# Kernel tuning notes

Measured on AMD Instinct MI355X. Metric: run time of the kernel, lower is better.

## Reference

```python
import jax, jax.numpy as jnp
import numpy as np

B, S, D, H = 4, 2048, 512, 4
HD = D // H
EPS = 1e-5


def layer_norm(x, gamma, beta):
    mu = jnp.mean(x, axis=-1, keepdims=True)
    var = jnp.mean(jnp.square(x - mu), axis=-1, keepdims=True)
    return (x - mu) * jax.lax.rsqrt(var + EPS) * gamma + beta


def setup_inputs() -> dict:
    key = jax.random.key(0)
    ks = jax.random.split(key, 16)
    s_in = 1.0 / np.sqrt(D)
    s_ex = 1.0 / np.sqrt(2 * D)
    return {
        "input_states": jax.random.normal(ks[0], (B, S, D), jnp.float32),
        "positions": jax.random.normal(ks[1], (B, S, 3), jnp.float32),
        "W_expand": jax.random.uniform(ks[2], (D, 2 * D), jnp.float32, -s_in, s_in),
        "b_expand": jax.random.uniform(ks[3], (2 * D,), jnp.float32, -s_in, s_in),
        "W_squeeze": jax.random.uniform(ks[4], (2 * D, D), jnp.float32, -s_ex, s_ex),
        "b_squeeze": jax.random.uniform(ks[5], (D,), jnp.float32, -s_ex, s_ex),
        "gamma": jnp.ones((D,), jnp.float32),
        "beta": jnp.zeros((D,), jnp.float32),
        "Wq": jax.random.uniform(ks[6], (D, D), jnp.float32, -s_in, s_in),
        "bq": jax.random.uniform(ks[7], (D,), jnp.float32, -s_in, s_in),
        "Wk": jax.random.uniform(ks[8], (D, D), jnp.float32, -s_in, s_in),
        "bk": jax.random.uniform(ks[9], (D,), jnp.float32, -s_in, s_in),
        "Wv": jax.random.uniform(ks[10], (D, D), jnp.float32, -s_in, s_in),
        "bv": jax.random.uniform(ks[11], (D,), jnp.float32, -s_in, s_in),
        "alpha": jnp.float32(0.1),
    }


def reference(input_states, positions, W_expand, b_expand, W_squeeze, b_squeeze,
              gamma, beta, Wq, bq, Wk, bk, Wv, bv, alpha):
    # FFN (expand -> relu -> squeeze) + residual + LayerNorm
    h = jax.nn.relu(input_states @ W_expand + b_expand)
    squeezed = h @ W_squeeze + b_squeeze
    se = layer_norm(input_states + squeezed, gamma, beta)

    # q/k/v projections, split heads: [B,H,S,HD]
    q = (se @ Wq + bq).reshape(B, S, H, HD).transpose(0, 2, 1, 3)
    k = (se @ Wk + bk).reshape(B, S, H, HD).transpose(0, 2, 1, 3)
    v = (se @ Wv + bv).reshape(B, S, H, HD).transpose(0, 2, 1, 3)

    scores = jnp.einsum('bhid,bhjd->bhij', q, k) / np.sqrt(HD)

    # squared pairwise distance bias: ||pi||^2 + ||pj||^2 - 2 pi.pj, broadcast over heads
    sq = jnp.sum(positions * positions, axis=-1)  # [B,S]
    dist2 = sq[:, :, None] + sq[:, None, :] - 2.0 * jnp.einsum('bic,bjc->bij', positions, positions)
    dist2 = jnp.maximum(dist2, 0.0)
    scores = scores - alpha * dist2[:, None, :, :]

    w = jax.nn.softmax(scores, axis=-1)
    ctx = jnp.einsum('bhij,bhjd->bhid', w, v)
    ctx = ctx.transpose(0, 2, 1, 3).reshape(B, S, D)

    # same LayerNorm params reused (self.norm applied twice in original)
    return layer_norm(se + ctx, gamma, beta)
```

## Files before the change

kernel.cpp:

```cpp
#include <hip/hip_runtime.h>

typedef __bf16 bf16_t;
typedef __attribute__((ext_vector_type(8))) __bf16 bf16x8;
typedef __attribute__((ext_vector_type(4))) __bf16 bf16x4;
typedef __attribute__((ext_vector_type(4))) float f32x4;
typedef __attribute__((ext_vector_type(16))) float f32x16;

constexpr int Bc = 4, Sc = 2048, Dc = 512, Hc = 4, HDc = 128;
constexpr int Mrows = Bc * Sc;

__device__ inline void gl2lds(const void* g, void* l) {
  __builtin_amdgcn_global_load_lds(
      (__attribute__((address_space(1))) void*)g,
      (__attribute__((address_space(3))) void*)l, 16, 0, 0);
}

__global__ __launch_bounds__(256) void prep_k(
    const float* __restrict__ X, bf16_t* __restrict__ xb,
    const float* __restrict__ pos, const float* __restrict__ alphap,
    float* __restrict__ pos2,
    const float* __restrict__ We, bf16_t* __restrict__ wtE,
    const float* __restrict__ Ws, bf16_t* __restrict__ wtS,
    const float* __restrict__ Wq, const float* __restrict__ Wk,
    const float* __restrict__ Wv, bf16_t* __restrict__ wtQKV) {
  const int bid = blockIdx.x;
  if (bid < 2048) {
    const long i = ((long)bid * 256 + threadIdx.x) * 8;
    const float4 a = *(const float4*)(X + i);
    const float4 c = *(const float4*)(X + i + 4);
    bf16x8 o;
    o[0] = (bf16_t)a.x; o[1] = (bf16_t)a.y; o[2] = (bf16_t)a.z; o[3] = (bf16_t)a.w;
    o[4] = (bf16_t)c.x; o[5] = (bf16_t)c.y; o[6] = (bf16_t)c.z; o[7] = (bf16_t)c.w;
    *(bf16x8*)(xb + i) = o;
    return;
  }
  if (bid < 2080) {
    const float aL = alphap[0] * 1.4426950408889634f;
    const int i = (bid - 2048) * 256 + threadIdx.x;
    const float x = pos[(long)i * 3], y = pos[(long)i * 3 + 1], z = pos[(long)i * 3 + 2];
    float4 o; o.x = x; o.y = y; o.z = z; o.w = -aL * (x * x + y * y + z * z);
    *(float4*)(pos2 + (long)i * 4) = o;
    return;
  }
  __shared__ float tile[32][33];
  const float* src; bf16_t* dst; int K, N, local;
  if (bid < 2592)      { src = We; dst = wtE; K = 512;  N = 1024; local = bid - 2080; }
  else if (bid < 3104) { src = Ws; dst = wtS; K = 1024; N = 512;  local = bid - 2592; }
  else if (bid < 3360) { src = Wq; dst = wtQKV;          K = 512; N = 512; local = bid - 3104; }
  else if (bid < 3616) { src = Wk; dst = wtQKV + 262144; K = 512; N = 512; local = bid - 3360; }
  else                 { src = Wv; dst = wtQKV + 524288; K = 512; N = 512; local = bid - 3616; }
  const int nb = N / 32;
  const int n0 = (local % nb) * 32, k0 = (local / nb) * 32;
  const int tx = threadIdx.x & 31, ty = threadIdx.x >> 5;
#pragma unroll
  for (int i = 0; i < 4; i++)
    tile[ty + i * 8][tx] = src[(long)(k0 + ty + i * 8) * N + n0 + tx];
  __syncthreads();
#pragma unroll
  for (int i = 0; i < 4; i++)
    dst[(long)(n0 + ty + i * 8) * K + k0 + tx] = (bf16_t)tile[tx][ty + i * 8];
}

template <int OMODE, int TN, int NB>
__global__ __launch_bounds__(256, (TN == 128) ? 2 : 3) void gemm128_k(
    const bf16_t* __restrict__ A, const bf16_t* __restrict__ Bt,
    const float* __restrict__ bias0, const float* __restrict__ bias1,
    const float* __restrict__ bias2, void* __restrict__ out0,
    void* __restrict__ out1, void* __restrict__ out2, int N, int K) {
  __shared__ bf16_t As[2][128 * 64];
  __shared__ bf16_t Bs[2][TN * 64];
  constexpr int MT = (TN == 128) ? 4 : 2;
  constexpr int BI = (TN == 128) ? 4 : 2;
  constexpr int MW = (TN == 128) ? 64 : 32;
  const int t = threadIdx.x;
  const int p = blockIdx.x;
  const int slot = p >> 3;
  const int by = (p & 7) + 8 * (slot / NB);
  const int bx = slot % NB;
  const int n0 = bx * TN, m0 = by * 128;
  const int lane = t & 63, wave = t >> 6;
  const int quad = lane >> 4, ln = lane & 15;
  const int wm = (TN == 128) ? (wave >> 1) : wave;
  const int wn = (TN == 128) ? (wave & 1) : 0;
  const int l8 = lane >> 3, g = lane & 7;
  const bf16_t* aseg = A + (long)(m0 + wave * 32 + l8) * K + (g ^ l8) * 8;
  const bf16_t* bseg = Bt + (long)(n0 + wave * (BI * 8) + l8) * K + (g ^ l8) * 8;
  auto stage = [&](int buf, int k0) {
#pragma unroll
    for (int i = 0; i < 4; i++)
      gl2lds(aseg + (long)i * 8 * K + k0, &As[buf][(wave * 32 + i * 8) * 64]);
#pragma unroll
    for (int i = 0; i < BI; i++)
      gl2lds(bseg + (long)i * 8 * K + k0, &Bs[buf][(wave * BI * 8 + i * 8) * 64]);
  };
  f32x4 acc[MT][4] = {};
  stage(0, 0);
  const int niter = K / 64;
  for (int it = 0; it < niter; it++) {
    const int cur = it & 1;
    __syncthreads();
    if (it + 1 < niter) stage(1 - cur, (it + 1) * 64);
#pragma unroll
    for (int kc = 0; kc < 2; kc++) {
      bf16x8 af[MT], bfr[4];
#pragma unroll
      for (int mt = 0; mt < MT; mt++)
        af[mt] = *(const bf16x8*)&As[cur][(wm * MW + mt * 16 + ln) * 64 +
                                          (((kc * 4 + quad) ^ (ln & 7)) * 8)];
#pragma unroll
      for (int nt = 0; nt < 4; nt++)
        bfr[nt] = *(const bf16x8*)&Bs[cur][(wn * 64 + nt * 16 + ln) * 64 +
                                           (((kc * 4 + quad) ^ (ln & 7)) * 8)];
#pragma unroll
      for (int mt = 0; mt < MT; mt++)
#pragma unroll
        for (int nt = 0; nt < 4; nt++)
          acc[mt][nt] = __builtin_amdgcn_mfma_f32_16x16x32_bf16(af[mt], bfr[nt],
                                                                acc[mt][nt], 0, 0, 0);
    }
  }
#pragma unroll
  for (int nt = 0; nt < 4; nt++) {
    const int gcol = n0 + wn * 64 + nt * 16 + ln;
    if constexpr (OMODE == 0 || OMODE == 1) {
      const float bv = bias0[gcol];
      bf16_t* o = (bf16_t*)out0;
#pragma unroll
      for (int mt = 0; mt < MT; mt++)
#pragma unroll
        for (int r = 0; r < 4; r++) {
          const int grow = m0 + wm * MW + mt * 16 + quad * 4 + r;
          float vv = acc[mt][nt][r] + bv;
          if constexpr (OMODE == 0) vv = vv > 0.f ? vv : 0.f;
          o[(long)grow * N + gcol] = (bf16_t)vv;
        }
    } else {
      const int which = gcol >> 9, n = gcol & 511;
      const int hh = n >> 7, hd = n & 127;
      const float bv = (which == 0 ? bias0 : which == 1 ? bias1 : bias2)[n];
      bf16_t* o = (bf16_t*)(which == 0 ? out0 : which == 1 ? out1 : out2);
#pragma unroll
      for (int mt = 0; mt < MT; mt++)
#pragma unroll
        for (int r = 0; r < 4; r++) {
          const int grow = m0 + wm * MW + mt * 16 + quad * 4 + r;
          const int b = grow >> 11, s = grow & 2047;
          const float vv = acc[mt][nt][r] + bv;
          long idx;
          if (which == 0) {
            idx = ((long)((b * Hc + hh) * Sc + s)) * HDc + hd;
          } else if (which == 1) {
            const int tt = s >> 6, kh = (s >> 5) & 1, key = s & 31;
            const int c = hd >> 4, lk = key + 32 * ((hd >> 3) & 1), j = hd & 7;
            idx = ((((long)((b * Hc + hh) * 32 + tt) * 2 + kh) * 8 + c) * 64 + lk) * 8 + j;
          } else {
            const int tt = s >> 6, ht2 = hd >> 5, kc = (s & 63) >> 4;
            const int lk = (hd & 31) + 32 * ((s >> 3) & 1), j = s & 7;
            idx = ((((long)((b * Hc + hh) * 32 + tt) * 4 + ht2) * 4 + kc) * 64 + lk) * 8 + j;
          }
          o[idx] = (bf16_t)vv;
        }
    }
  }
}

template <int AF32, int OF32>
__global__ __launch_bounds__(256) void ln_k(const void* __restrict__ xa,
                                            const bf16_t* __restrict__ xb,
                                            const float* __restrict__ gamma,
                                            const float* __restrict__ beta,
                                            void* __restrict__ out) {
  const int wave = threadIdx.x >> 6, lane = threadIdx.x & 63;
  const long row = (long)blockIdx.x * 4 + wave;
  const int col0 = lane * 8;
  float vv[8];
  float s = 0.f, s2 = 0.f;
  const bf16x8 vb = *(const bf16x8*)(xb + row * Dc + col0);
  if constexpr (AF32) {
    const float* a = (const float*)xa + row * Dc + col0;
    const float4 a0 = *(const float4*)a;
    const float4 a1 = *(const float4*)(a + 4);
    const float xs[8] = {a0.x, a0.y, a0.z, a0.w, a1.x, a1.y, a1.z, a1.w};
#pragma unroll
    for (int j = 0; j < 8; j++) vv[j] = xs[j] + (float)vb[j];
  } else {
    const bf16x8 va = *(const bf16x8*)((const bf16_t*)xa + row * Dc + col0);
#pragma unroll
    for (int j = 0; j < 8; j++) vv[j] = (float)va[j] + (float)vb[j];
  }
#pragma unroll
  for (int j = 0; j < 8; j++) { s += vv[j]; s2 += vv[j] * vv[j]; }
#pragma unroll
  for (int off = 1; off < 64; off <<= 1) {
    s += __shfl_xor(s, off, 64);
    s2 += __shfl_xor(s2, off, 64);
  }
  const float mu = s * (1.f / Dc);
  const float var = s2 * (1.f / Dc) - mu * mu;
  const float rstd = rsqrtf(var + 1e-5f);
  const float4 g0 = *(const float4*)(gamma + col0);
  const float4 g1 = *(const float4*)(gamma + col0 + 4);
  const float4 b0 = *(const float4*)(beta + col0);
  const float4 b1 = *(const float4*)(beta + col0 + 4);
  const float gs[8] = {g0.x, g0.y, g0.z, g0.w, g1.x, g1.y, g1.z, g1.w};
  const float bs[8] = {b0.x, b0.y, b0.z, b0.w, b1.x, b1.y, b1.z, b1.w};
  if constexpr (OF32) {
    float* o = (float*)out + row * Dc + col0;
    float4 o0, o1;
    o0.x = (vv[0] - mu) * rstd * gs[0] + bs[0];
    o0.y = (vv[1] - mu) * rstd * gs[1] + bs[1];
    o0.z = (vv[2] - mu) * rstd * gs[2] + bs[2];
    o0.w = (vv[3] - mu) * rstd * gs[3] + bs[3];
    o1.x = (vv[4] - mu) * rstd * gs[4] + bs[4];
    o1.y = (vv[5] - mu) * rstd * gs[5] + bs[5];
    o1.z = (vv[6] - mu) * rstd * gs[6] + bs[6];
    o1.w = (vv[7] - mu) * rstd * gs[7] + bs[7];
    *(float4*)o = o0; *(float4*)(o + 4) = o1;
  } else {
    bf16x8 ob;
#pragma unroll
    for (int j = 0; j < 8; j++) ob[j] = (bf16_t)((vv[j] - mu) * rstd * gs[j] + bs[j]);
    *(bf16x8*)((bf16_t*)out + row * Dc + col0) = ob;
  }
}

__global__ __launch_bounds__(256, 2) void attn_k(const bf16_t* __restrict__ q,
                                                 const bf16_t* __restrict__ Kg,
                                                 const bf16_t* __restrict__ Vg,
                                                 const float* __restrict__ pos2,
                                                 const float* __restrict__ alphap,
                                                 bf16_t* __restrict__ ctx) {
  __shared__ bf16_t Ks[2][8192];
  __shared__ bf16_t Vts[2][8192];
  __shared__ float pk4[2][64][4];
  __shared__ bf16_t Ps[4][1024];
  __shared__ float RsD[4][32];
  const int t = threadIdx.x;
  const int p = blockIdx.x;
  const int qt = (p >> 3) & 31;
  const int gg = (p & 7) + 8 * (p >> 8);
  const int h = gg & 3, b = gg >> 2;
  const int q0 = qt * 64;
  const int wave = t >> 6, lane = t & 63;
  const int l31 = lane & 31, hb = lane >> 5;
  const int rh = wave & 1, kh = wave >> 1;
  const float l2e = 1.4426950408889634f;
  const float scale_l2 = l2e * 0.08838834764831845f;
  const float aL = alphap[0] * l2e;

  bf16x8 qf[8];
  const long qrow = (long)((b * Hc + h) * Sc + q0 + rh * 32 + l31);
#pragma unroll
  for (int c = 0; c < 8; c++)
    qf[c] = *(const bf16x8*)(q + qrow * HDc + c * 16 + hb * 8);
  float pqx, pqy, pqz;
  {
    const float4 pv = *(const float4*)(pos2 + (long)(b * Sc + q0 + rh * 32 + l31) * 4);
    pqx = 2.f * aL * pv.x; pqy = 2.f * aL * pv.y; pqz = 2.f * aL * pv.z;
  }

  const bf16_t* ktile = Kg + (long)((b * Hc + h) * 32) * 8192 + lane * 8;
  const bf16_t* vtile = Vg + (long)((b * Hc + h) * 32) * 8192 + lane * 8;
  const float* pcur = pos2 + (long)b * Sc * 4 + lane * 4;
  auto stage = [&](int buf) {
#pragma unroll
    for (int i = 0; i < 4; i++)
      gl2lds(ktile + (wave * 4 + i) * 512, &Ks[buf][(wave * 4 + i) * 512]);
#pragma unroll
    for (int i = 0; i < 4; i++)
      gl2lds(vtile + (wave * 4 + i) * 512, &Vts[buf][(wave * 4 + i) * 512]);
    if (wave == 0) gl2lds(pcur, &pk4[buf][0][0]);
  };
  stage(0);
  ktile += 8192; vtile += 8192; pcur += 256;

  float rsl = 0.f;
  f32x16 accT[4] = {};
  bf16_t* pwbase = &Ps[wave][l31 * 8 + 4 * hb];

  for (int kt = 0; kt < Sc / 64; kt++) {
    const int cur = kt & 1;
    __syncthreads();
    if (kt < Sc / 64 - 1) {
      stage(1 - cur);
      ktile += 8192; vtile += 8192; pcur += 256;
    }
    f32x16 sacc = {};
#pragma unroll
    for (int c = 0; c < 8; c++) {
      const bf16x8 kf = *(const bf16x8*)&Ks[cur][(kh * 8 + c) * 512 + lane * 8];
      sacc = __builtin_amdgcn_mfma_f32_32x32x16_bf16(kf, qf[c], sacc, 0, 0, 0);
    }
#pragma unroll
    for (int g2 = 0; g2 < 4; g2++) {
      bf16x4 pq4;
#pragma unroll
      for (int r0 = 0; r0 < 4; r0++) {
        const int kp = r0 + 4 * hb + 8 * g2;
        const float4 pv = *(const float4*)&pk4[cur][kh * 32 + kp][0];
        const float bias = __builtin_fmaf(pqx, pv.x,
                           __builtin_fmaf(pqy, pv.y,
                           __builtin_fmaf(pqz, pv.z, pv.w)));
        const float pe = __builtin_amdgcn_exp2f(
            __builtin_fmaf(sacc[g2 * 4 + r0], scale_l2, bias));
        rsl += pe;
        pq4[r0] = (bf16_t)pe;
      }
      *(bf16x4*)(pwbase + (g2 >> 1) * 512 + (g2 & 1) * 256) = pq4;
    }
    const bf16x8 pf0 = *(const bf16x8*)&Ps[wave][lane * 8];
    const bf16x8 pf1 = *(const bf16x8*)&Ps[wave][512 + lane * 8];
#pragma unroll
    for (int ht = 0; ht < 4; ht++) {
      const bf16x8 v0 = *(const bf16x8*)&Vts[cur][(ht * 4 + kh * 2 + 0) * 512 + lane * 8];
      accT[ht] = __builtin_amdgcn_mfma_f32_32x32x16_bf16(v0, pf0, accT[ht], 0, 0, 0);
      const bf16x8 v1 = *(const bf16x8*)&Vts[cur][(ht * 4 + kh * 2 + 1) * 512 + lane * 8];
      accT[ht] = __builtin_amdgcn_mfma_f32_32x32x16_bf16(v1, pf1, accT[ht], 0, 0, 0);
    }
  }
  __syncthreads();

  rsl += __shfl_xor(rsl, 32, 64);
  if (hb == 0) RsD[wave][l31] = rsl;
  float* Oc = (float*)&Ks[0][0];
  if (kh == 1) {
#pragma unroll
    for (int ht = 0; ht < 4; ht++)
#pragma unroll
      for (int r = 0; r < 16; r++) {
        const int hdp = (r & 3) + 8 * (r >> 2) + 4 * hb;
        Oc[(ht * 32 + hdp) * 64 + rh * 32 + l31] = accT[ht][r];
      }
  }
  __syncthreads();
  if (kh == 0) {
    const float rinv = 1.f / (RsD[wave][l31] + RsD[wave + 2][l31]);
    const long orow = (long)(b * Sc + q0 + rh * 32 + l31);
#pragma unroll
    for (int ht = 0; ht < 4; ht++)
#pragma unroll
      for (int g2 = 0; g2 < 4; g2++) {
        bf16x4 ov;
#pragma unroll
        for (int r0 = 0; r0 < 4; r0++) {
          const int hdp = r0 + 8 * g2 + 4 * hb;
          ov[r0] = (bf16_t)((accT[ht][g2 * 4 + r0] +
                             Oc[(ht * 32 + hdp) * 64 + rh * 32 + l31]) * rinv);
        }
        *(bf16x4*)(ctx + orow * Dc + h * HDc + ht * 32 + 8 * g2 + 4 * hb) = ov;
      }
  }
}

constexpr size_t SQB_OFF = 0;
constexpr size_t SEB_OFF = 8388608;
constexpr size_t Q_OFF = 16777216;
constexpr size_t K_OFF = 25165824;
constexpr size_t V_OFF = 33554432;
constexpr size_t XB_OFF = Q_OFF;
constexpr size_t H_OFF = K_OFF;
constexpr size_t POS2_OFF = 41943040;
constexpr size_t WTE_OFF = POS2_OFF + 131072;
constexpr size_t WTS_OFF = WTE_OFF + 1048576;
constexpr size_t WTQKV_OFF = WTS_OFF + 1048576;

extern "C" void kernel_launch(void* const* d_in, const int* in_sizes, int n_in,
                              void* d_out, int out_size, void* d_ws, size_t ws_size,
                              hipStream_t stream) {
  const float* X = (const float*)d_in[0];
  const float* pos = (const float*)d_in[1];
  const float* W_expand = (const float*)d_in[2];
  const float* b_expand = (const float*)d_in[3];
  const float* W_squeeze = (const float*)d_in[4];
  const float* b_squeeze = (const float*)d_in[5];
  const float* gamma = (const float*)d_in[6];
  const float* beta = (const float*)d_in[7];
  const float* Wq = (const float*)d_in[8];
  const float* bq = (const float*)d_in[9];
  const float* Wk = (const float*)d_in[10];
  const float* bk = (const float*)d_in[11];
  const float* Wv = (const float*)d_in[12];
  const float* bv = (const float*)d_in[13];
  const float* alphap = (const float*)d_in[14];

  char* ws = (char*)d_ws;
  bf16_t* sqb = (bf16_t*)(ws + SQB_OFF);
  bf16_t* ctxb = (bf16_t*)(ws + SQB_OFF);
  bf16_t* seb = (bf16_t*)(ws + SEB_OFF);
  float* pos2 = (float*)(ws + POS2_OFF);
  bf16_t* qb = (bf16_t*)(ws + Q_OFF);
  bf16_t* kb = (bf16_t*)(ws + K_OFF);
  bf16_t* vb = (bf16_t*)(ws + V_OFF);
  bf16_t* xbb = (bf16_t*)(ws + XB_OFF);
  bf16_t* hb = (bf16_t*)(ws + H_OFF);
  bf16_t* wtE = (bf16_t*)(ws + WTE_OFF);
  bf16_t* wtS = (bf16_t*)(ws + WTS_OFF);
  bf16_t* wtQKV = (bf16_t*)(ws + WTQKV_OFF);

  prep_k<<<3872, 256, 0, stream>>>(X, xbb, pos, alphap, pos2,
                                   W_expand, wtE, W_squeeze, wtS, Wq, Wk, Wv, wtQKV);
  gemm128_k<0, 128, 8><<<512, 256, 0, stream>>>(
      xbb, wtE, b_expand, nullptr, nullptr, hb, nullptr, nullptr, 1024, 512);
  gemm128_k<1, 64, 8><<<512, 256, 0, stream>>>(
      hb, wtS, b_squeeze, nullptr, nullptr, sqb, nullptr, nullptr, 512, 1024);
  ln_k<1, 0><<<Mrows / 4, 256, 0, stream>>>(X, sqb, gamma, beta, seb);
  gemm128_k<2, 128, 12><<<768, 256, 0, stream>>>(
      seb, wtQKV, bq, bk, bv, qb, kb, vb, 1536, 512);
  attn_k<<<512, 256, 0, stream>>>(qb, kb, vb, pos2, alphap, ctxb);
  ln_k<0, 1><<<Mrows / 4, 256, 0, stream>>>(seb, ctxb, gamma, beta, (float*)d_out);

  (void)in_sizes; (void)n_in; (void)out_size; (void)ws_size;
}
```

Baseline: 222.2 us.

## Fold distance bias into QK MFMA via augmented bf16 position vectors

Builds augmented bf16 query and key vectors from positions, pre-scaled so one extra 32x32x16 MFMA per tile produces the alpha-weighted squared-distance bias inside the score accumulator. This removes the per-element scalar FMA chain and the fp32 position LDS reads from the softmax loop. It also splits the QK accumulation into two chains to expose MFMA parallelism. The cost is bf16 rounding of positions and of the -alpha*|p|^2 term, which loses accuracy in the bias, plus some extra workspace and global traffic.

```diff
diff --git a/kernel.cpp b/kernel.cpp
--- a/kernel.cpp
+++ b/kernel.cpp
@@ -18,7 +18,7 @@
 __global__ __launch_bounds__(256) void prep_k(
     const float* __restrict__ X, bf16_t* __restrict__ xb,
     const float* __restrict__ pos, const float* __restrict__ alphap,
-    float* __restrict__ pos2,
+    bf16_t* __restrict__ Qbg, bf16_t* __restrict__ Kbg,
     const float* __restrict__ We, bf16_t* __restrict__ wtE,
     const float* __restrict__ Ws, bf16_t* __restrict__ wtS,
     const float* __restrict__ Wq, const float* __restrict__ Wk,
@@ -35,11 +35,21 @@
     return;
   }
   if (bid < 2080) {
-    const float aL = alphap[0] * 1.4426950408889634f;
+    const float ap = alphap[0] * 11.313708498984761f;
     const int i = (bid - 2048) * 256 + threadIdx.x;
+    const int b = i >> 11, s = i & 2047;
     const float x = pos[(long)i * 3], y = pos[(long)i * 3 + 1], z = pos[(long)i * 3 + 2];
-    float4 o; o.x = x; o.y = y; o.z = z; o.w = -aL * (x * x + y * y + z * z);
-    *(float4*)(pos2 + (long)i * 4) = o;
+    const float m2 = -ap * (x * x + y * y + z * z);
+    bf16x8 qlo = {}, klo = {}, zer = {};
+    qlo[0] = (bf16_t)(2.f * ap * x); qlo[1] = (bf16_t)(2.f * ap * y);
+    qlo[2] = (bf16_t)(2.f * ap * z); qlo[3] = (bf16_t)1.0f;
+    klo[0] = (bf16_t)x; klo[1] = (bf16_t)y; klo[2] = (bf16_t)z; klo[3] = (bf16_t)m2;
+    *(bf16x8*)(Qbg + (long)i * 16) = qlo;
+    *(bf16x8*)(Qbg + (long)i * 16 + 8) = zer;
+    const int t = s >> 6, kh = (s >> 5) & 1, key = s & 31;
+    const long kb = ((long)(b * 32 + t) * 2 + kh) * 512 + key * 8;
+    *(bf16x8*)(Kbg + kb) = klo;
+    *(bf16x8*)(Kbg + kb + 256) = zer;
     return;
   }
   __shared__ float tile[32][33];
@@ -227,12 +237,12 @@
 __global__ __launch_bounds__(256, 2) void attn_k(const bf16_t* __restrict__ q,
                                                  const bf16_t* __restrict__ Kg,
                                                  const bf16_t* __restrict__ Vg,
-                                                 const float* __restrict__ pos2,
-                                                 const float* __restrict__ alphap,
+                                                 const bf16_t* __restrict__ Qbg,
+                                                 const bf16_t* __restrict__ Kbg,
                                                  bf16_t* __restrict__ ctx) {
   __shared__ bf16_t Ks[2][8192];
   __shared__ bf16_t Vts[2][8192];
-  __shared__ float pk4[2][64][4];
+  __shared__ bf16_t Kb[2][1024];
   __shared__ bf16_t Ps[4][1024];
   __shared__ float RsD[4][32];
   const int t = threadIdx.x;
@@ -244,24 +254,18 @@
   const int wave = t >> 6, lane = t & 63;
   const int l31 = lane & 31, hb = lane >> 5;
   const int rh = wave & 1, kh = wave >> 1;
-  const float l2e = 1.4426950408889634f;
-  const float scale_l2 = l2e * 0.08838834764831845f;
-  const float aL = alphap[0] * l2e;
-
-  bf16x8 qf[8];
+  const float scale_l2 = 1.4426950408889634f * 0.08838834764831845f;
+
+  bf16x8 qf[8], qbf;
   const long qrow = (long)((b * Hc + h) * Sc + q0 + rh * 32 + l31);
 #pragma unroll
   for (int c = 0; c < 8; c++)
     qf[c] = *(const bf16x8*)(q + qrow * HDc + c * 16 + hb * 8);
-  float pqx, pqy, pqz;
-  {
-    const float4 pv = *(const float4*)(pos2 + (long)(b * Sc + q0 + rh * 32 + l31) * 4);
-    pqx = 2.f * aL * pv.x; pqy = 2.f * aL * pv.y; pqz = 2.f * aL * pv.z;
-  }
+  qbf = *(const bf16x8*)(Qbg + (long)(b * Sc + q0 + rh * 32 + l31) * 16 + hb * 8);
 
   const bf16_t* ktile = Kg + (long)((b * Hc + h) * 32) * 8192 + lane * 8;
   const bf16_t* vtile = Vg + (long)((b * Hc + h) * 32) * 8192 + lane * 8;
-  const float* pcur = pos2 + (long)b * Sc * 4 + lane * 4;
+  const bf16_t* kbtile = Kbg + (long)(b * 32) * 1024 + lane * 8;
   auto stage = [&](int buf) {
 #pragma unroll
     for (int i = 0; i < 4; i++)
@@ -269,10 +273,10 @@
 #pragma unroll
     for (int i = 0; i < 4; i++)
       gl2lds(vtile + (wave * 4 + i) * 512, &Vts[buf][(wave * 4 + i) * 512]);
-    if (wave == 0) gl2lds(pcur, &pk4[buf][0][0]);
+    if (wave < 2) gl2lds(kbtile + wave * 512, &Kb[buf][wave * 512]);
   };
   stage(0);
-  ktile += 8192; vtile += 8192; pcur += 256;
+  ktile += 8192; vtile += 8192; kbtile += 1024;
 
   float rsl = 0.f;
   f32x16 accT[4] = {};
@@ -283,26 +287,30 @@
     __syncthreads();
     if (kt < Sc / 64 - 1) {
       stage(1 - cur);
-      ktile += 8192; vtile += 8192; pcur += 256;
-    }
-    f32x16 sacc = {};
-#pragma unroll
-    for (int c = 0; c < 8; c++) {
+      ktile += 8192; vtile += 8192; kbtile += 1024;
+    }
+    f32x16 sa = {}, sb = {};
+#pragma unroll
+    for (int c = 0; c < 4; c++) {
       const bf16x8 kf = *(const bf16x8*)&Ks[cur][(kh * 8 + c) * 512 + lane * 8];
-      sacc = __builtin_amdgcn_mfma_f32_32x32x16_bf16(kf, qf[c], sacc, 0, 0, 0);
-    }
+      sa = __builtin_amdgcn_mfma_f32_32x32x16_bf16(kf, qf[c], sa, 0, 0, 0);
+    }
+#pragma unroll
+    for (int c = 4; c < 8; c++) {
+      const bf16x8 kf = *(const bf16x8*)&Ks[cur][(kh * 8 + c) * 512 + lane * 8];
+      sb = __builtin_amdgcn_mfma_f32_32x32x16_bf16(kf, qf[c], sb, 0, 0, 0);
+    }
+    {
+      const bf16x8 kbf = *(const bf16x8*)&Kb[cur][kh * 512 + lane * 8];
+      sb = __builtin_amdgcn_mfma_f32_32x32x16_bf16(kbf, qbf, sb, 0, 0, 0);
+    }
+    const f32x16 sacc = sa + sb;
 #pragma unroll
     for (int g2 = 0; g2 < 4; g2++) {
       bf16x4 pq4;
 #pragma unroll
       for (int r0 = 0; r0 < 4; r0++) {
-        const int kp = r0 + 4 * hb + 8 * g2;
-        const float4 pv = *(const float4*)&pk4[cur][kh * 32 + kp][0];
-        const float bias = __builtin_fmaf(pqx, pv.x,
-                           __builtin_fmaf(pqy, pv.y,
-                           __builtin_fmaf(pqz, pv.z, pv.w)));
-        const float pe = __builtin_amdgcn_exp2f(
-            __builtin_fmaf(sacc[g2 * 4 + r0], scale_l2, bias));
+        const float pe = __builtin_amdgcn_exp2f(sacc[g2 * 4 + r0] * scale_l2);
         rsl += pe;
         pq4[r0] = (bf16_t)pe;
       }
@@ -359,8 +367,9 @@
 constexpr size_t V_OFF = 33554432;
 constexpr size_t XB_OFF = Q_OFF;
 constexpr size_t H_OFF = K_OFF;
-constexpr size_t POS2_OFF = 41943040;
-constexpr size_t WTE_OFF = POS2_OFF + 131072;
+constexpr size_t QBG_OFF = 41943040;
+constexpr size_t KBG_OFF = QBG_OFF + 262144;
+constexpr size_t WTE_OFF = KBG_OFF + 262144;
 constexpr size_t WTS_OFF = WTE_OFF + 1048576;
 constexpr size_t WTQKV_OFF = WTS_OFF + 1048576;
 
@@ -387,7 +396,8 @@
   bf16_t* sqb = (bf16_t*)(ws + SQB_OFF);
   bf16_t* ctxb = (bf16_t*)(ws + SQB_OFF);
   bf16_t* seb = (bf16_t*)(ws + SEB_OFF);
-  float* pos2 = (float*)(ws + POS2_OFF);
+  bf16_t* qbg = (bf16_t*)(ws + QBG_OFF);
+  bf16_t* kbg = (bf16_t*)(ws + KBG_OFF);
   bf16_t* qb = (bf16_t*)(ws + Q_OFF);
   bf16_t* kb = (bf16_t*)(ws + K_OFF);
   bf16_t* vb = (bf16_t*)(ws + V_OFF);
@@ -397,7 +407,7 @@
   bf16_t* wtS = (bf16_t*)(ws + WTS_OFF);
   bf16_t* wtQKV = (bf16_t*)(ws + WTQKV_OFF);
 
-  prep_k<<<3872, 256, 0, stream>>>(X, xbb, pos, alphap, pos2,
+  prep_k<<<3872, 256, 0, stream>>>(X, xbb, pos, alphap, qbg, kbg,
                                    W_expand, wtE, W_squeeze, wtS, Wq, Wk, Wv, wtQKV);
   gemm128_k<0, 128, 8><<<512, 256, 0, stream>>>(
       xbb, wtE, b_expand, nullptr, nullptr, hb, nullptr, nullptr, 1024, 512);
@@ -406,7 +416,7 @@
   ln_k<1, 0><<<Mrows / 4, 256, 0, stream>>>(X, sqb, gamma, beta, seb);
   gemm128_k<2, 128, 12><<<768, 256, 0, stream>>>(
       seb, wtQKV, bq, bk, bv, qb, kb, vb, 1536, 512);
-  attn_k<<<512, 256, 0, stream>>>(qb, kb, vb, pos2, alphap, ctxb);
+  attn_k<<<512, 256, 0, stream>>>(qb, kb, vb, qbg, kbg, ctxb);
   ln_k<0, 1><<<Mrows / 4, 256, 0, stream>>>(seb, ctxb, gamma, beta, (float*)d_out);
 
   (void)in_sizes; (void)n_in; (void)out_size; (void)ws_size;
```

New measurement: 214.7 us. -3.4%, faster.
